# Performance work log

Measured on AMD Instinct MI355X. Metric: run time of the kernel, lower is better.

## Reference

```python
import jax, jax.numpy as jnp
import numpy as np

B, S, D = 2, 2048, 1024
HEADS, HEAD_DIM = 16, 64

def setup_inputs() -> dict:
    key = jax.random.key(0)
    ks = jax.random.split(key, 5)
    sc = 0.02
    return {
        "hidden_states": jax.random.normal(ks[0], (B, S, D), jnp.float32),
        "Wq": jax.random.normal(ks[1], (D, HEADS * HEAD_DIM), jnp.float32) * sc,
        "Wk": jax.random.normal(ks[2], (D, HEADS * HEAD_DIM), jnp.float32) * sc,
        "Wv": jax.random.normal(ks[3], (D, HEADS * HEAD_DIM), jnp.float32) * sc,
        "Wo": jax.random.normal(ks[4], (HEADS * HEAD_DIM, D), jnp.float32) * sc,
        "bo": jnp.zeros((D,), jnp.float32),
    }

def reference(hidden_states, Wq, Wk, Wv, Wo, bo):
    b, s, _ = hidden_states.shape
    # QKV projections (no bias, as in diffusers Attention defaults)
    q = (hidden_states @ Wq).reshape(b, s, HEADS, HEAD_DIM).transpose(0, 2, 1, 3)
    k = (hidden_states @ Wk).reshape(b, s, HEADS, HEAD_DIM).transpose(0, 2, 1, 3)
    v = (hidden_states @ Wv).reshape(b, s, HEADS, HEAD_DIM).transpose(0, 2, 1, 3)
    scale = 1.0 / jnp.sqrt(jnp.asarray(HEAD_DIM, hidden_states.dtype))
    scores = jnp.einsum('bhqd,bhkd->bhqk', q, k) * scale  # full NxN scores
    attn = jax.nn.softmax(scores, axis=-1)
    out = jnp.einsum('bhqk,bhkd->bhqd', attn, v)
    out = out.transpose(0, 2, 1, 3).reshape(b, s, HEADS * HEAD_DIM)
    return out @ Wo + bo
```

## Files before the change

### kernel.cpp

```cpp
#include <hip/hip_runtime.h>

#define B_ 2
#define S_ 2048
#define D_ 1024
#define H_ 16
#define HD_ 64
#define M_ (B_ * S_)

typedef __attribute__((ext_vector_type(4))) float f32x4;
typedef __attribute__((ext_vector_type(16))) float f32x16;
typedef __attribute__((ext_vector_type(8))) short s16x8;
typedef unsigned short u16;
typedef unsigned int u32;

#define QSCALE 0.1803368801111204f

__device__ __forceinline__ u16 f2bf(float f) {
  unsigned u = __float_as_uint(f);
  u += 0x7fffu + ((u >> 16) & 1u);
  return (u16)(u >> 16);
}

__device__ __forceinline__ u32 cvtpk_bf16(float lo, float hi) {
  u32 r;
  asm("v_cvt_pk_bf16_f32 %0, %1, %2" : "=v"(r) : "v"(lo), "v"(hi));
  return r;
}

__device__ __forceinline__ void g2lds16(const u16* g, u16* l) {
  __builtin_amdgcn_global_load_lds((const __attribute__((address_space(1))) u32*)(g),
                                   (__attribute__((address_space(3))) u32*)(l), 16, 0, 0);
}

__global__ __launch_bounds__(256) void prep_kernel(
    const float* __restrict__ X, const float* __restrict__ Wq,
    const float* __restrict__ Wk, const float* __restrict__ Wv,
    const float* __restrict__ Wo, u16* __restrict__ Xb, u16* __restrict__ Wt0) {
  __shared__ float tile[32][33];
  const int id = blockIdx.x;
  if (id < 4096) {
    int i = (id * 256 + threadIdx.x) * 4;
    const float4 v = *(const float4*)(X + i);
    ushort4 o;
    o.x = f2bf(v.x); o.y = f2bf(v.y); o.z = f2bf(v.z); o.w = f2bf(v.w);
    *(ushort4*)(Xb + i) = o;
    return;
  }
  const int id2 = id - 4096;
  const int z = id2 >> 10;
  const float* W = (z == 0) ? Wq : (z == 1) ? Wk : (z == 2) ? Wv : Wo;
  u16* Wt = Wt0 + (size_t)z * (D_ * D_);
  const float sc = (z == 0) ? QSCALE : 1.0f;
  const int tx = threadIdx.x & 31, ty = threadIdx.x >> 5;
  const int c0 = (id2 & 31) * 32, r0 = ((id2 >> 5) & 31) * 32;
#pragma unroll
  for (int j = 0; j < 32; j += 8)
    tile[ty + j][tx] = W[(size_t)(r0 + ty + j) * D_ + c0 + tx];
  __syncthreads();
#pragma unroll
  for (int j = 0; j < 32; j += 8)
    Wt[(size_t)(c0 + ty + j) * D_ + r0 + tx] = f2bf(tile[tx][ty + j] * sc);
}

__global__ __launch_bounds__(256) void gemm_qkv_kernel(
    const u16* __restrict__ Xb, const u16* __restrict__ WqT,
    const u16* __restrict__ WkT, const u16* __restrict__ WvT,
    u16* __restrict__ Qb, u16* __restrict__ Kb, u16* __restrict__ Vt) {
  __shared__ u16 As[2][128 * 32];
  __shared__ u16 Bs[2][128 * 32];
  const int tid = threadIdx.x;
  const int lane = tid & 63, wid = tid >> 6;
  const int wr = wid >> 1, wc = wid & 1;
  const int l15 = lane & 15, l4 = lane >> 4;
  const int bm = blockIdx.x * 128;
  const int bn128 = blockIdx.y;
  const int sel = bn128 >> 3;
  const u16* Wt = (sel == 0) ? WqT : (sel == 1) ? WkT : WvT;
  const int bn = (bn128 & 7) * 128;
  const int r0 = lane >> 2;
  const int c0 = lane & 3;

#define GSTAGE(buf, kt)                                                          \
  do {                                                                           \
    _Pragma("unroll") for (int j = 0; j < 2; ++j) {                              \
      const int row = (wid * 2 + j) * 16 + r0;                                   \
      g2lds16(Xb + (size_t)(bm + row) * D_ + (kt) + c0 * 8,                      \
              &As[buf][(wid * 2 + j) * 512]);                                    \
      g2lds16(Wt + (size_t)(bn + row) * D_ + (kt) + c0 * 8,                      \
              &Bs[buf][(wid * 2 + j) * 512]);                                    \
    }                                                                            \
  } while (0)

  f32x4 acc[4][4] = {};
  GSTAGE(0, 0);
  __syncthreads();
  int cur = 0;
  for (int kt = 0; kt < D_; kt += 32) {
    GSTAGE(cur ^ 1, (kt + 32) & (D_ - 1));
    s16x8 af[4], bfr[4];
#pragma unroll
    for (int i = 0; i < 4; ++i) af[i] = *(const s16x8*)&As[cur][(wr * 64 + i * 16 + l15) * 32 + l4 * 8];
#pragma unroll
    for (int j = 0; j < 4; ++j) bfr[j] = *(const s16x8*)&Bs[cur][(wc * 64 + j * 16 + l15) * 32 + l4 * 8];
#pragma unroll
    for (int i = 0; i < 4; ++i)
#pragma unroll
      for (int j = 0; j < 4; ++j)
        acc[i][j] = __builtin_amdgcn_mfma_f32_16x16x32_bf16(af[i], bfr[j], acc[i][j], 0, 0, 0);
    __syncthreads();
    cur ^= 1;
  }
#undef GSTAGE
#pragma unroll
  for (int i = 0; i < 4; ++i)
#pragma unroll
    for (int j = 0; j < 4; ++j)
#pragma unroll
      for (int r = 0; r < 4; ++r) {
        int m = bm + wr * 64 + i * 16 + l4 * 4 + r;
        int n = bn + wc * 64 + j * 16 + l15;
        int bb = m >> 11, s = m & (S_ - 1);
        int h = n >> 6, d = n & 63;
        u16 v = f2bf(acc[i][j][r]);
        size_t bhsel = (size_t)bb * H_ + h;
        if (sel == 0)      Qb[(bhsel * S_ + s) * HD_ + d] = v;
        else if (sel == 1) Kb[(bhsel * S_ + s) * HD_ + d] = v;
        else               Vt[(bhsel * HD_ + d) * S_ + s] = v;
      }
}

__global__ __launch_bounds__(512, 4) void attn_kernel(
    const u16* __restrict__ Qb, const u16* __restrict__ Kb,
    const u16* __restrict__ Vt, u16* __restrict__ Ob) {
  __shared__ char smem_raw[65536];
  typedef u16 (*lds_t)[2][4096];
  lds_t Ks = (lds_t)smem_raw;
  lds_t Vs = (lds_t)(smem_raw + 32768);
  const int tid = threadIdx.x;
  const int lane = tid & 63, wid = tid >> 6;
  const int qg = wid & 3, half = wid >> 2;
  const int l31 = lane & 31, hi = lane >> 5;
  const int id = blockIdx.x;
  const int bh = (id & 7) * 4 + ((id >> 3) >> 4);
  const int qx = (id >> 3) & 15;
  const size_t kbase = (size_t)bh * S_ * HD_;
  const size_t vbase = (size_t)bh * HD_ * S_;
  const int q0 = qx * 128 + qg * 32;
  const int r0 = lane >> 3;
  const int cs = ((lane & 7) ^ r0) * 8;
  const int kv0 = half << 10;

#define STAGE(buf, kvv)                                                          \
  do {                                                                           \
    _Pragma("unroll") for (int j = 0; j < 2; ++j) {                              \
      const int row = (qg * 2 + j) * 8 + r0;                                     \
      g2lds16(Kb + kbase + (size_t)((kvv) + row) * HD_ + cs,                     \
              &Ks[half][buf][(qg * 2 + j) * 512]);                               \
      g2lds16(Vt + vbase + (size_t)row * S_ + (kvv) + cs,                        \
              &Vs[half][buf][(qg * 2 + j) * 512]);                               \
    }                                                                            \
  } while (0)

  STAGE(0, kv0);

  s16x8 aq[4];
#pragma unroll
  for (int kc = 0; kc < 4; ++kc)
    aq[kc] = *(const s16x8*)(Qb + kbase + (size_t)(q0 + l31) * HD_ + kc * 16 + hi * 8);

  f32x16 acc0 = {}, acc1 = {};
  float ls = 0.f;

  __syncthreads();

  for (int t = 0; t < 16; ++t) {
    const int buf = t & 1;
    STAGE(buf ^ 1, kv0 + (((t + 1) & 15) << 6));

    f32x16 s0 = {}, s1 = {};
    __builtin_amdgcn_s_setprio(1);
#pragma unroll
    for (int kc = 0; kc < 4; ++kc) {
      const int ch = ((kc * 2 + hi) ^ (l31 & 7)) * 8;
      const s16x8 ka0 = *(const s16x8*)&Ks[half][buf][(l31) * 64 + ch];
      const s16x8 ka1 = *(const s16x8*)&Ks[half][buf][(32 + l31) * 64 + ch];
      s0 = __builtin_amdgcn_mfma_f32_32x32x16_bf16(ka0, aq[kc], s0, 0, 0, 0);
      s1 = __builtin_amdgcn_mfma_f32_32x32x16_bf16(ka1, aq[kc], s1, 0, 0, 0);
    }
    __builtin_amdgcn_s_setprio(0);

    float t0 = 0.f, t1 = 0.f;
#pragma unroll
    for (int r = 0; r < 16; ++r) {
      s0[r] = __builtin_amdgcn_exp2f(s0[r]);
      s1[r] = __builtin_amdgcn_exp2f(s1[r]);
      t0 += s0[r];
      t1 += s1[r];
    }
    ls += t0 + t1;

    s16x8 pa[4];
#pragma unroll
    for (int c = 0; c < 4; ++c) {
      const int rr = (c & 1) * 8;
      u32 a0, a1, b0, b1;
      if (c < 2) {
        a0 = cvtpk_bf16(s0[rr + 0], s0[rr + 1]);
        a1 = cvtpk_bf16(s0[rr + 2], s0[rr + 3]);
        b0 = cvtpk_bf16(s0[rr + 4], s0[rr + 5]);
        b1 = cvtpk_bf16(s0[rr + 6], s0[rr + 7]);
      } else {
        a0 = cvtpk_bf16(s1[rr + 0], s1[rr + 1]);
        a1 = cvtpk_bf16(s1[rr + 2], s1[rr + 3]);
        b0 = cvtpk_bf16(s1[rr + 4], s1[rr + 5]);
        b1 = cvtpk_bf16(s1[rr + 6], s1[rr + 7]);
      }
      asm volatile("v_permlane32_swap_b32 %0, %1" : "+v"(a0), "+v"(b0));
      asm volatile("v_permlane32_swap_b32 %0, %1" : "+v"(a1), "+v"(b1));
      union { u32 u[4]; s16x8 v; } pk;
      pk.u[0] = a0; pk.u[1] = a1; pk.u[2] = b0; pk.u[3] = b1;
      pa[c] = pk.v;
    }

    __builtin_amdgcn_s_setprio(1);
#pragma unroll
    for (int c = 0; c < 4; ++c) {
      const int ch = ((c * 2 + hi) ^ (l31 & 7)) * 8;
      const s16x8 vb0 = *(const s16x8*)&Vs[half][buf][(l31) * 64 + ch];
      const s16x8 vb1 = *(const s16x8*)&Vs[half][buf][(32 + l31) * 64 + ch];
      acc0 = __builtin_amdgcn_mfma_f32_32x32x16_bf16(pa[c], vb0, acc0, 0, 0, 0);
      acc1 = __builtin_amdgcn_mfma_f32_32x32x16_bf16(pa[c], vb1, acc1, 0, 0, 0);
    }
    __builtin_amdgcn_s_setprio(0);

    __syncthreads();
  }
#undef STAGE

  float (*MB)[64][33] = (float(*)[64][33])smem_raw;
  if (half) {
#pragma unroll
    for (int r = 0; r < 16; ++r) {
      MB[qg][lane][r] = acc0[r];
      MB[qg][lane][16 + r] = acc1[r];
    }
    MB[qg][lane][32] = ls;
  }
  __syncthreads();
  if (!half) {
#pragma unroll
    for (int r = 0; r < 16; ++r) {
      acc0[r] += MB[qg][lane][r];
      acc1[r] += MB[qg][lane][16 + r];
    }
    ls += MB[qg][lane][32];
    ls += __shfl_xor(ls, 32);
    const int bb = bh >> 4, h = bh & 15;
#pragma unroll
    for (int r = 0; r < 16; ++r) {
      const int qrow = (r & 3) + 8 * (r >> 2) + 4 * hi;
      const float rinv = 1.0f / __shfl(ls, qrow);
      const int q = q0 + qrow;
      Ob[(size_t)(bb * S_ + q) * (H_ * HD_) + h * HD_ + l31] = f2bf(acc0[r] * rinv);
      Ob[(size_t)(bb * S_ + q) * (H_ * HD_) + h * HD_ + 32 + l31] = f2bf(acc1[r] * rinv);
    }
  }
}

__global__ __launch_bounds__(256) void gemm_o_kernel(
    const u16* __restrict__ A, const u16* __restrict__ Bt,
    const float* __restrict__ bias, float* __restrict__ C) {
  __shared__ u16 As[2][128 * 32];
  __shared__ u16 Bs[2][128 * 32];
  const int tid = threadIdx.x;
  const int lane = tid & 63, wid = tid >> 6;
  const int wr = wid >> 1, wc = wid & 1;
  const int l15 = lane & 15, l4 = lane >> 4;
  const int bm = blockIdx.x * 128;
  const int bn = blockIdx.y * 128;
  const int r0 = lane >> 2;
  const int c0 = lane & 3;

#define GSTAGE(buf, kt)                                                          \
  do {                                                                           \
    _Pragma("unroll") for (int j = 0; j < 2; ++j) {                              \
      const int row = (wid * 2 + j) * 16 + r0;                                   \
      g2lds16(A + (size_t)(bm + row) * D_ + (kt) + c0 * 8,                       \
              &As[buf][(wid * 2 + j) * 512]);                                    \
      g2lds16(Bt + (size_t)(bn + row) * D_ + (kt) + c0 * 8,                      \
              &Bs[buf][(wid * 2 + j) * 512]);                                    \
    }                                                                            \
  } while (0)

  f32x4 acc[4][4] = {};
  GSTAGE(0, 0);
  __syncthreads();
  int cur = 0;
  for (int kt = 0; kt < D_; kt += 32) {
    GSTAGE(cur ^ 1, (kt + 32) & (D_ - 1));
    s16x8 af[4], bfr[4];
#pragma unroll
    for (int i = 0; i < 4; ++i) af[i] = *(const s16x8*)&As[cur][(wr * 64 + i * 16 + l15) * 32 + l4 * 8];
#pragma unroll
    for (int j = 0; j < 4; ++j) bfr[j] = *(const s16x8*)&Bs[cur][(wc * 64 + j * 16 + l15) * 32 + l4 * 8];
#pragma unroll
    for (int i = 0; i < 4; ++i)
#pragma unroll
      for (int j = 0; j < 4; ++j)
        acc[i][j] = __builtin_amdgcn_mfma_f32_16x16x32_bf16(af[i], bfr[j], acc[i][j], 0, 0, 0);
    __syncthreads();
    cur ^= 1;
  }
#undef GSTAGE
#pragma unroll
  for (int i = 0; i < 4; ++i)
#pragma unroll
    for (int j = 0; j < 4; ++j)
#pragma unroll
      for (int r = 0; r < 4; ++r) {
        int m = bm + wr * 64 + i * 16 + l4 * 4 + r;
        int n = bn + wc * 64 + j * 16 + l15;
        C[(size_t)m * D_ + n] = acc[i][j][r] + bias[n];
      }
}

extern "C" void kernel_launch(void* const* d_in, const int* in_sizes, int n_in,
                              void* d_out, int out_size, void* d_ws, size_t ws_size,
                              hipStream_t stream) {
  const float* X  = (const float*)d_in[0];
  const float* Wq = (const float*)d_in[1];
  const float* Wk = (const float*)d_in[2];
  const float* Wv = (const float*)d_in[3];
  const float* Wo = (const float*)d_in[4];
  const float* bo = (const float*)d_in[5];
  float* out = (float*)d_out;

  char* w = (char*)d_ws;
  u16* Xb  = (u16*)(w);
  u16* WT  = (u16*)(w + (8u << 20));
  u16* WqT = WT;
  u16* WkT = WT + (1u << 20);
  u16* WvT = WT + (2u << 20);
  u16* WoT = WT + (3u << 20);
  u16* Qb  = (u16*)(w + (16u << 20));
  u16* Kb  = (u16*)(w + (24u << 20));
  u16* Vt  = (u16*)(w + (32u << 20));
  u16* Ob  = (u16*)(w + (40u << 20));

  prep_kernel<<<8192, 256, 0, stream>>>(X, Wq, Wk, Wv, Wo, Xb, WT);
  gemm_qkv_kernel<<<dim3(32, 24), 256, 0, stream>>>(Xb, WqT, WkT, WvT, Qb, Kb, Vt);
  attn_kernel<<<512, 512, 0, stream>>>(Qb, Kb, Vt, Ob);
  gemm_o_kernel<<<dim3(32, 8), 256, 0, stream>>>(Ob, WoT, bo, out);
}
```

Measured before the change: 116.9 us.

## Compute softmax row sums via MFMA with ones and swizzle GEMM block mapping

The attention kernel drops the per-lane VALU sum of exponentials. It adds an extra MFMA of P against an all-ones bf16 vector, so the row sums land in the same layout as the output accumulator, which removes the shuffles in the epilogue. Both GEMM kernels switch to a 1D grid with a block-index swizzle that spreads consecutive blocks across XCDs and changes tile order for L2 locality. The LDS swizzle offsets are also hoisted into registers. The cost is one extra MFMA per four PV MFMAs, a larger merge buffer in shared memory, and row sums built from bf16-rounded probabilities.

```diff
diff --git a/kernel.cpp b/kernel.cpp
--- a/kernel.cpp
+++ b/kernel.cpp
@@ -72,8 +72,9 @@
   const int lane = tid & 63, wid = tid >> 6;
   const int wr = wid >> 1, wc = wid & 1;
   const int l15 = lane & 15, l4 = lane >> 4;
-  const int bm = blockIdx.x * 128;
-  const int bn128 = blockIdx.y;
+  const int swz = (blockIdx.x & 7) * 96 + (blockIdx.x >> 3);
+  const int bm = (swz & 31) * 128;
+  const int bn128 = swz >> 5;
   const int sel = bn128 >> 3;
   const u16* Wt = (sel == 0) ? WqT : (sel == 1) ? WkT : WvT;
   const int bn = (bn128 & 7) * 128;
@@ -168,8 +169,14 @@
   for (int kc = 0; kc < 4; ++kc)
     aq[kc] = *(const s16x8*)(Qb + kbase + (size_t)(q0 + l31) * HD_ + kc * 16 + hi * 8);
 
-  f32x16 acc0 = {}, acc1 = {};
-  float ls = 0.f;
+  const short one_bf = (short)0x3F80;
+  const s16x8 ones8 = {one_bf, one_bf, one_bf, one_bf, one_bf, one_bf, one_bf, one_bf};
+
+  f32x16 acc0 = {}, acc1 = {}, lsacc = {};
+
+  int choff[4];
+#pragma unroll
+  for (int c = 0; c < 4; ++c) choff[c] = ((c * 2 + hi) ^ (l31 & 7)) * 8;
 
   __syncthreads();
 
@@ -181,23 +188,18 @@
     __builtin_amdgcn_s_setprio(1);
 #pragma unroll
     for (int kc = 0; kc < 4; ++kc) {
-      const int ch = ((kc * 2 + hi) ^ (l31 & 7)) * 8;
-      const s16x8 ka0 = *(const s16x8*)&Ks[half][buf][(l31) * 64 + ch];
-      const s16x8 ka1 = *(const s16x8*)&Ks[half][buf][(32 + l31) * 64 + ch];
+      const s16x8 ka0 = *(const s16x8*)&Ks[half][buf][(l31) * 64 + choff[kc]];
+      const s16x8 ka1 = *(const s16x8*)&Ks[half][buf][(32 + l31) * 64 + choff[kc]];
       s0 = __builtin_amdgcn_mfma_f32_32x32x16_bf16(ka0, aq[kc], s0, 0, 0, 0);
       s1 = __builtin_amdgcn_mfma_f32_32x32x16_bf16(ka1, aq[kc], s1, 0, 0, 0);
     }
     __builtin_amdgcn_s_setprio(0);
 
-    float t0 = 0.f, t1 = 0.f;
 #pragma unroll
     for (int r = 0; r < 16; ++r) {
       s0[r] = __builtin_amdgcn_exp2f(s0[r]);
       s1[r] = __builtin_amdgcn_exp2f(s1[r]);
-      t0 += s0[r];
-      t1 += s1[r];
-    }
-    ls += t0 + t1;
+    }
 
     s16x8 pa[4];
 #pragma unroll
@@ -225,11 +227,11 @@
     __builtin_amdgcn_s_setprio(1);
 #pragma unroll
     for (int c = 0; c < 4; ++c) {
-      const int ch = ((c * 2 + hi) ^ (l31 & 7)) * 8;
-      const s16x8 vb0 = *(const s16x8*)&Vs[half][buf][(l31) * 64 + ch];
-      const s16x8 vb1 = *(const s16x8*)&Vs[half][buf][(32 + l31) * 64 + ch];
+      const s16x8 vb0 = *(const s16x8*)&Vs[half][buf][(l31) * 64 + choff[c]];
+      const s16x8 vb1 = *(const s16x8*)&Vs[half][buf][(32 + l31) * 64 + choff[c]];
       acc0 = __builtin_amdgcn_mfma_f32_32x32x16_bf16(pa[c], vb0, acc0, 0, 0, 0);
       acc1 = __builtin_amdgcn_mfma_f32_32x32x16_bf16(pa[c], vb1, acc1, 0, 0, 0);
+      lsacc = __builtin_amdgcn_mfma_f32_32x32x16_bf16(pa[c], ones8, lsacc, 0, 0, 0);
     }
     __builtin_amdgcn_s_setprio(0);
 
@@ -237,32 +239,27 @@
   }
 #undef STAGE
 
-  float (*MB)[64][33] = (float(*)[64][33])smem_raw;
+  float (*MB)[64][49] = (float(*)[64][49])smem_raw;
   if (half) {
 #pragma unroll
     for (int r = 0; r < 16; ++r) {
       MB[qg][lane][r] = acc0[r];
       MB[qg][lane][16 + r] = acc1[r];
-    }
-    MB[qg][lane][32] = ls;
+      MB[qg][lane][32 + r] = lsacc[r];
+    }
   }
   __syncthreads();
   if (!half) {
+    const int bb = bh >> 4, h = bh & 15;
 #pragma unroll
     for (int r = 0; r < 16; ++r) {
-      acc0[r] += MB[qg][lane][r];
-      acc1[r] += MB[qg][lane][16 + r];
-    }
-    ls += MB[qg][lane][32];
-    ls += __shfl_xor(ls, 32);
-    const int bb = bh >> 4, h = bh & 15;
-#pragma unroll
-    for (int r = 0; r < 16; ++r) {
+      const float o0 = acc0[r] + MB[qg][lane][r];
+      const float o1 = acc1[r] + MB[qg][lane][16 + r];
+      const float rinv = 1.0f / (lsacc[r] + MB[qg][lane][32 + r]);
       const int qrow = (r & 3) + 8 * (r >> 2) + 4 * hi;
-      const float rinv = 1.0f / __shfl(ls, qrow);
       const int q = q0 + qrow;
-      Ob[(size_t)(bb * S_ + q) * (H_ * HD_) + h * HD_ + l31] = f2bf(acc0[r] * rinv);
-      Ob[(size_t)(bb * S_ + q) * (H_ * HD_) + h * HD_ + 32 + l31] = f2bf(acc1[r] * rinv);
+      Ob[(size_t)(bb * S_ + q) * (H_ * HD_) + h * HD_ + l31] = f2bf(o0 * rinv);
+      Ob[(size_t)(bb * S_ + q) * (H_ * HD_) + h * HD_ + 32 + l31] = f2bf(o1 * rinv);
     }
   }
 }
@@ -276,8 +273,9 @@
   const int lane = tid & 63, wid = tid >> 6;
   const int wr = wid >> 1, wc = wid & 1;
   const int l15 = lane & 15, l4 = lane >> 4;
-  const int bm = blockIdx.x * 128;
-  const int bn = blockIdx.y * 128;
+  const int swz = (blockIdx.x & 7) * 32 + (blockIdx.x >> 3);
+  const int bm = (swz & 31) * 128;
+  const int bn = (swz >> 5) * 128;
   const int r0 = lane >> 2;
   const int c0 = lane & 3;
 
@@ -348,7 +346,7 @@
   u16* Ob  = (u16*)(w + (40u << 20));
 
   prep_kernel<<<8192, 256, 0, stream>>>(X, Wq, Wk, Wv, Wo, Xb, WT);
-  gemm_qkv_kernel<<<dim3(32, 24), 256, 0, stream>>>(Xb, WqT, WkT, WvT, Qb, Kb, Vt);
+  gemm_qkv_kernel<<<768, 256, 0, stream>>>(Xb, WqT, WkT, WvT, Qb, Kb, Vt);
   attn_kernel<<<512, 512, 0, stream>>>(Qb, Kb, Vt, Ob);
-  gemm_o_kernel<<<dim3(32, 8), 256, 0, stream>>>(Ob, WoT, bo, out);
-}
+  gemm_o_kernel<<<256, 256, 0, stream>>>(Ob, WoT, bo, out);
+}
```

Result: slower. 129.0 us (+10.4%).

## Fuse X fp32-to-bf16 conversion into QKV GEMM and widen N tile to 256

Applied to the files above, without the earlier changes.

Drops the separate conversion pass that wrote a bf16 copy of the hidden states. The QKV GEMM now loads fp32 X directly into registers, converts it with packed bf16 conversion instructions, and writes it to LDS. The GEMM block also grows to 512 threads with a 128x256 tile, so each converted A tile is reused across more output columns. This saves one global write/read round trip of X. The cost is register-based A staging instead of async global-to-LDS loads, half as many GEMM blocks, and more LDS per block.

```diff
diff --git a/kernel.cpp b/kernel.cpp
--- a/kernel.cpp
+++ b/kernel.cpp
@@ -33,26 +33,17 @@
 }
 
 __global__ __launch_bounds__(256) void prep_kernel(
-    const float* __restrict__ X, const float* __restrict__ Wq,
-    const float* __restrict__ Wk, const float* __restrict__ Wv,
-    const float* __restrict__ Wo, u16* __restrict__ Xb, u16* __restrict__ Wt0) {
+    const float* __restrict__ Wq, const float* __restrict__ Wk,
+    const float* __restrict__ Wv, const float* __restrict__ Wo,
+    u16* __restrict__ Wt0) {
   __shared__ float tile[32][33];
   const int id = blockIdx.x;
-  if (id < 4096) {
-    int i = (id * 256 + threadIdx.x) * 4;
-    const float4 v = *(const float4*)(X + i);
-    ushort4 o;
-    o.x = f2bf(v.x); o.y = f2bf(v.y); o.z = f2bf(v.z); o.w = f2bf(v.w);
-    *(ushort4*)(Xb + i) = o;
-    return;
-  }
-  const int id2 = id - 4096;
-  const int z = id2 >> 10;
+  const int z = id >> 10;
   const float* W = (z == 0) ? Wq : (z == 1) ? Wk : (z == 2) ? Wv : Wo;
   u16* Wt = Wt0 + (size_t)z * (D_ * D_);
   const float sc = (z == 0) ? QSCALE : 1.0f;
   const int tx = threadIdx.x & 31, ty = threadIdx.x >> 5;
-  const int c0 = (id2 & 31) * 32, r0 = ((id2 >> 5) & 31) * 32;
+  const int c0 = (id & 31) * 32, r0 = ((id >> 5) & 31) * 32;
 #pragma unroll
   for (int j = 0; j < 32; j += 8)
     tile[ty + j][tx] = W[(size_t)(r0 + ty + j) * D_ + c0 + tx];
@@ -62,41 +53,55 @@
     Wt[(size_t)(c0 + ty + j) * D_ + r0 + tx] = f2bf(tile[tx][ty + j] * sc);
 }
 
-__global__ __launch_bounds__(256) void gemm_qkv_kernel(
-    const u16* __restrict__ Xb, const u16* __restrict__ WqT,
+__global__ __launch_bounds__(512) void gemm_qkv_kernel(
+    const float* __restrict__ X, const u16* __restrict__ WqT,
     const u16* __restrict__ WkT, const u16* __restrict__ WvT,
     u16* __restrict__ Qb, u16* __restrict__ Kb, u16* __restrict__ Vt) {
   __shared__ u16 As[2][128 * 32];
-  __shared__ u16 Bs[2][128 * 32];
+  __shared__ u16 Bs[2][256 * 32];
   const int tid = threadIdx.x;
   const int lane = tid & 63, wid = tid >> 6;
-  const int wr = wid >> 1, wc = wid & 1;
+  const int wr = wid >> 2, wc = wid & 3;
   const int l15 = lane & 15, l4 = lane >> 4;
   const int bm = blockIdx.x * 128;
-  const int bn128 = blockIdx.y;
-  const int sel = bn128 >> 3;
+  const int strip = blockIdx.y;
+  const int sel = strip >> 2;
   const u16* Wt = (sel == 0) ? WqT : (sel == 1) ? WkT : WvT;
-  const int bn = (bn128 & 7) * 128;
-  const int r0 = lane >> 2;
-  const int c0 = lane & 3;
-
-#define GSTAGE(buf, kt)                                                          \
+  const int bnp = (strip & 3) * 256;
+  const int arow = tid >> 2, ac = tid & 3;
+  const float* Xa = X + (size_t)(bm + arow) * D_ + ac * 8;
+  const int brow0 = wid * 16 + (lane >> 2), bc = lane & 3;
+
+#define STAGE_B(buf, kt)                                                         \
   do {                                                                           \
-    _Pragma("unroll") for (int j = 0; j < 2; ++j) {                              \
-      const int row = (wid * 2 + j) * 16 + r0;                                   \
-      g2lds16(Xb + (size_t)(bm + row) * D_ + (kt) + c0 * 8,                      \
-              &As[buf][(wid * 2 + j) * 512]);                                    \
-      g2lds16(Wt + (size_t)(bn + row) * D_ + (kt) + c0 * 8,                      \
-              &Bs[buf][(wid * 2 + j) * 512]);                                    \
-    }                                                                            \
+    _Pragma("unroll") for (int j = 0; j < 2; ++j)                                \
+      g2lds16(Wt + (size_t)(bnp + brow0 + j * 128) * D_ + (kt) + bc * 8,         \
+              &Bs[buf][wid * 512 + j * 4096]);                                   \
   } while (0)
 
+#define LOAD_A(kt)                                                               \
+  xa = *(const float4*)(Xa + (kt));                                              \
+  xb = *(const float4*)(Xa + (kt) + 4)
+
+#define WRITE_A(buf)                                                             \
+  do {                                                                           \
+    union { u32 u[4]; s16x8 v; } pk;                                             \
+    pk.u[0] = cvtpk_bf16(xa.x, xa.y); pk.u[1] = cvtpk_bf16(xa.z, xa.w);          \
+    pk.u[2] = cvtpk_bf16(xb.x, xb.y); pk.u[3] = cvtpk_bf16(xb.z, xb.w);          \
+    *(s16x8*)&As[buf][tid * 8] = pk.v;                                           \
+  } while (0)
+
+  float4 xa, xb;
   f32x4 acc[4][4] = {};
-  GSTAGE(0, 0);
+  LOAD_A(0);
+  STAGE_B(0, 0);
+  WRITE_A(0);
   __syncthreads();
   int cur = 0;
   for (int kt = 0; kt < D_; kt += 32) {
-    GSTAGE(cur ^ 1, (kt + 32) & (D_ - 1));
+    const int nkt = (kt + 32) & (D_ - 1);
+    LOAD_A(nkt);
+    STAGE_B(cur ^ 1, nkt);
     s16x8 af[4], bfr[4];
 #pragma unroll
     for (int i = 0; i < 4; ++i) af[i] = *(const s16x8*)&As[cur][(wr * 64 + i * 16 + l15) * 32 + l4 * 8];
@@ -107,10 +112,13 @@
 #pragma unroll
       for (int j = 0; j < 4; ++j)
         acc[i][j] = __builtin_amdgcn_mfma_f32_16x16x32_bf16(af[i], bfr[j], acc[i][j], 0, 0, 0);
+    WRITE_A(cur ^ 1);
     __syncthreads();
     cur ^= 1;
   }
-#undef GSTAGE
+#undef STAGE_B
+#undef LOAD_A
+#undef WRITE_A
 #pragma unroll
   for (int i = 0; i < 4; ++i)
 #pragma unroll
@@ -118,7 +126,7 @@
 #pragma unroll
       for (int r = 0; r < 4; ++r) {
         int m = bm + wr * 64 + i * 16 + l4 * 4 + r;
-        int n = bn + wc * 64 + j * 16 + l15;
+        int n = bnp + wc * 64 + j * 16 + l15;
         int bb = m >> 11, s = m & (S_ - 1);
         int h = n >> 6, d = n & 63;
         u16 v = f2bf(acc[i][j][r]);
@@ -336,7 +344,6 @@
   float* out = (float*)d_out;
 
   char* w = (char*)d_ws;
-  u16* Xb  = (u16*)(w);
   u16* WT  = (u16*)(w + (8u << 20));
   u16* WqT = WT;
   u16* WkT = WT + (1u << 20);
@@ -347,8 +354,8 @@
   u16* Vt  = (u16*)(w + (32u << 20));
   u16* Ob  = (u16*)(w + (40u << 20));
 
-  prep_kernel<<<8192, 256, 0, stream>>>(X, Wq, Wk, Wv, Wo, Xb, WT);
-  gemm_qkv_kernel<<<dim3(32, 24), 256, 0, stream>>>(Xb, WqT, WkT, WvT, Qb, Kb, Vt);
+  prep_kernel<<<4096, 256, 0, stream>>>(Wq, Wk, Wv, Wo, WT);
+  gemm_qkv_kernel<<<dim3(32, 12), 512, 0, stream>>>(X, WqT, WkT, WvT, Qb, Kb, Vt);
   attn_kernel<<<512, 512, 0, stream>>>(Qb, Kb, Vt, Ob);
   gemm_o_kernel<<<dim3(32, 8), 256, 0, stream>>>(Ob, WoT, bo, out);
 }
```

After: 125.7 us. +7.6%, slower.

## Split attention KV halves into separate blocks, merge partials in output GEMM

Applied to the files above, without the earlier changes.

The attention kernel now launches 1024 blocks of 256 threads, each handling one KV half, instead of 512 blocks of 512 threads that reduced both halves through LDS. Each half writes unnormalized bf16 partial outputs and row sums to global buffers. The output-projection GEMM loads both partials, sums them, normalizes by the combined row sum and packs the result into LDS as its A operand. This removes the in-block reduction barrier and raises block-level parallelism, but adds an extra partial-output round trip through global memory and extra bf16 rounding. It also reuses the Xb buffer for the second partial.

```diff
diff --git a/kernel.cpp b/kernel.cpp
--- a/kernel.cpp
+++ b/kernel.cpp
@@ -19,6 +19,10 @@
   unsigned u = __float_as_uint(f);
   u += 0x7fffu + ((u >> 16) & 1u);
   return (u16)(u >> 16);
+}
+
+__device__ __forceinline__ float bf2f(short s) {
+  return __uint_as_float(((u32)(unsigned short)s) << 16);
 }
 
 __device__ __forceinline__ u32 cvtpk_bf16(float lo, float hi) {
@@ -129,23 +133,24 @@
       }
 }
 
-__global__ __launch_bounds__(512, 4) void attn_kernel(
+__global__ __launch_bounds__(256, 4) void attn_kernel(
     const u16* __restrict__ Qb, const u16* __restrict__ Kb,
-    const u16* __restrict__ Vt, u16* __restrict__ Ob) {
-  __shared__ char smem_raw[65536];
-  typedef u16 (*lds_t)[2][4096];
-  lds_t Ks = (lds_t)smem_raw;
-  lds_t Vs = (lds_t)(smem_raw + 32768);
+    const u16* __restrict__ Vt, u16* __restrict__ P0, u16* __restrict__ P1,
+    float* __restrict__ ls0, float* __restrict__ ls1) {
+  __shared__ u16 Ks[2][4096];
+  __shared__ u16 Vs[2][4096];
   const int tid = threadIdx.x;
   const int lane = tid & 63, wid = tid >> 6;
-  const int qg = wid & 3, half = wid >> 2;
   const int l31 = lane & 31, hi = lane >> 5;
   const int id = blockIdx.x;
-  const int bh = (id & 7) * 4 + ((id >> 3) >> 4);
-  const int qx = (id >> 3) & 15;
+  const int rr_ = id >> 3;
+  const int bh = (id & 7) * 4 + (rr_ >> 5);
+  const int sub = rr_ & 31;
+  const int half = sub >> 4;
+  const int qx = sub & 15;
   const size_t kbase = (size_t)bh * S_ * HD_;
   const size_t vbase = (size_t)bh * HD_ * S_;
-  const int q0 = qx * 128 + qg * 32;
+  const int q0 = qx * 128 + wid * 32;
   const int r0 = lane >> 3;
   const int cs = ((lane & 7) ^ r0) * 8;
   const int kv0 = half << 10;
@@ -153,11 +158,11 @@
 #define STAGE(buf, kvv)                                                          \
   do {                                                                           \
     _Pragma("unroll") for (int j = 0; j < 2; ++j) {                              \
-      const int row = (qg * 2 + j) * 8 + r0;                                     \
+      const int row = (wid * 2 + j) * 8 + r0;                                    \
       g2lds16(Kb + kbase + (size_t)((kvv) + row) * HD_ + cs,                     \
-              &Ks[half][buf][(qg * 2 + j) * 512]);                               \
+              &Ks[buf][(wid * 2 + j) * 512]);                                    \
       g2lds16(Vt + vbase + (size_t)row * S_ + (kvv) + cs,                        \
-              &Vs[half][buf][(qg * 2 + j) * 512]);                               \
+              &Vs[buf][(wid * 2 + j) * 512]);                                    \
     }                                                                            \
   } while (0)
 
@@ -182,8 +187,8 @@
 #pragma unroll
     for (int kc = 0; kc < 4; ++kc) {
       const int ch = ((kc * 2 + hi) ^ (l31 & 7)) * 8;
-      const s16x8 ka0 = *(const s16x8*)&Ks[half][buf][(l31) * 64 + ch];
-      const s16x8 ka1 = *(const s16x8*)&Ks[half][buf][(32 + l31) * 64 + ch];
+      const s16x8 ka0 = *(const s16x8*)&Ks[buf][(l31) * 64 + ch];
+      const s16x8 ka1 = *(const s16x8*)&Ks[buf][(32 + l31) * 64 + ch];
       s0 = __builtin_amdgcn_mfma_f32_32x32x16_bf16(ka0, aq[kc], s0, 0, 0, 0);
       s1 = __builtin_amdgcn_mfma_f32_32x32x16_bf16(ka1, aq[kc], s1, 0, 0, 0);
     }
@@ -226,8 +231,8 @@
 #pragma unroll
     for (int c = 0; c < 4; ++c) {
       const int ch = ((c * 2 + hi) ^ (l31 & 7)) * 8;
-      const s16x8 vb0 = *(const s16x8*)&Vs[half][buf][(l31) * 64 + ch];
-      const s16x8 vb1 = *(const s16x8*)&Vs[half][buf][(32 + l31) * 64 + ch];
+      const s16x8 vb0 = *(const s16x8*)&Vs[buf][(l31) * 64 + ch];
+      const s16x8 vb1 = *(const s16x8*)&Vs[buf][(32 + l31) * 64 + ch];
       acc0 = __builtin_amdgcn_mfma_f32_32x32x16_bf16(pa[c], vb0, acc0, 0, 0, 0);
       acc1 = __builtin_amdgcn_mfma_f32_32x32x16_bf16(pa[c], vb1, acc1, 0, 0, 0);
     }
@@ -237,39 +242,25 @@
   }
 #undef STAGE
 
-  float (*MB)[64][33] = (float(*)[64][33])smem_raw;
-  if (half) {
-#pragma unroll
-    for (int r = 0; r < 16; ++r) {
-      MB[qg][lane][r] = acc0[r];
-      MB[qg][lane][16 + r] = acc1[r];
-    }
-    MB[qg][lane][32] = ls;
-  }
-  __syncthreads();
-  if (!half) {
-#pragma unroll
-    for (int r = 0; r < 16; ++r) {
-      acc0[r] += MB[qg][lane][r];
-      acc1[r] += MB[qg][lane][16 + r];
-    }
-    ls += MB[qg][lane][32];
-    ls += __shfl_xor(ls, 32);
-    const int bb = bh >> 4, h = bh & 15;
-#pragma unroll
-    for (int r = 0; r < 16; ++r) {
-      const int qrow = (r & 3) + 8 * (r >> 2) + 4 * hi;
-      const float rinv = 1.0f / __shfl(ls, qrow);
-      const int q = q0 + qrow;
-      Ob[(size_t)(bb * S_ + q) * (H_ * HD_) + h * HD_ + l31] = f2bf(acc0[r] * rinv);
-      Ob[(size_t)(bb * S_ + q) * (H_ * HD_) + h * HD_ + 32 + l31] = f2bf(acc1[r] * rinv);
-    }
+  ls += __shfl_xor(ls, 32);
+  const int bb = bh >> 4, h = bh & 15;
+  u16* P = half ? P1 : P0;
+  float* LS = half ? ls1 : ls0;
+  if (hi == 0) LS[(size_t)(bb * S_ + q0 + l31) * H_ + h] = ls;
+#pragma unroll
+  for (int r = 0; r < 16; ++r) {
+    const int qrow = (r & 3) + 8 * (r >> 2) + 4 * hi;
+    const int q = q0 + qrow;
+    P[(size_t)(bb * S_ + q) * (H_ * HD_) + h * HD_ + l31] = f2bf(acc0[r]);
+    P[(size_t)(bb * S_ + q) * (H_ * HD_) + h * HD_ + 32 + l31] = f2bf(acc1[r]);
   }
 }
 
 __global__ __launch_bounds__(256) void gemm_o_kernel(
-    const u16* __restrict__ A, const u16* __restrict__ Bt,
-    const float* __restrict__ bias, float* __restrict__ C) {
+    const u16* __restrict__ P0, const u16* __restrict__ P1,
+    const float* __restrict__ ls0, const float* __restrict__ ls1,
+    const u16* __restrict__ Bt, const float* __restrict__ bias,
+    float* __restrict__ C) {
   __shared__ u16 As[2][128 * 32];
   __shared__ u16 Bs[2][128 * 32];
   const int tid = threadIdx.x;
@@ -280,24 +271,54 @@
   const int bn = blockIdx.y * 128;
   const int r0 = lane >> 2;
   const int c0 = lane & 3;
-
-#define GSTAGE(buf, kt)                                                          \
+  const int arow0 = (wid * 2) * 16 + r0, arow1 = (wid * 2 + 1) * 16 + r0;
+
+#define STAGE_B(buf, kt)                                                         \
   do {                                                                           \
     _Pragma("unroll") for (int j = 0; j < 2; ++j) {                              \
       const int row = (wid * 2 + j) * 16 + r0;                                   \
-      g2lds16(A + (size_t)(bm + row) * D_ + (kt) + c0 * 8,                       \
-              &As[buf][(wid * 2 + j) * 512]);                                    \
       g2lds16(Bt + (size_t)(bn + row) * D_ + (kt) + c0 * 8,                      \
               &Bs[buf][(wid * 2 + j) * 512]);                                    \
     }                                                                            \
   } while (0)
 
+#define LOAD_M(kt)                                                               \
+  do {                                                                           \
+    const int col = (kt) + c0 * 8, hh = col >> 6;                                \
+    ma0 = *(const s16x8*)&P0[(size_t)(bm + arow0) * D_ + col];                   \
+    mb0 = *(const s16x8*)&P1[(size_t)(bm + arow0) * D_ + col];                   \
+    ma1 = *(const s16x8*)&P0[(size_t)(bm + arow1) * D_ + col];                   \
+    mb1 = *(const s16x8*)&P1[(size_t)(bm + arow1) * D_ + col];                   \
+    lsv0 = ls0[(size_t)(bm + arow0) * H_ + hh] + ls1[(size_t)(bm + arow0) * H_ + hh]; \
+    lsv1 = ls0[(size_t)(bm + arow1) * H_ + hh] + ls1[(size_t)(bm + arow1) * H_ + hh]; \
+  } while (0)
+
+#define WRITE_M(buf)                                                             \
+  do {                                                                           \
+    const float ri0 = 1.0f / lsv0, ri1 = 1.0f / lsv1;                            \
+    union { u32 u[4]; s16x8 v; } pk0, pk1;                                       \
+    _Pragma("unroll") for (int e = 0; e < 4; ++e) {                              \
+      pk0.u[e] = cvtpk_bf16((bf2f(ma0[2 * e]) + bf2f(mb0[2 * e])) * ri0,         \
+                            (bf2f(ma0[2 * e + 1]) + bf2f(mb0[2 * e + 1])) * ri0);\
+      pk1.u[e] = cvtpk_bf16((bf2f(ma1[2 * e]) + bf2f(mb1[2 * e])) * ri1,         \
+                            (bf2f(ma1[2 * e + 1]) + bf2f(mb1[2 * e + 1])) * ri1);\
+    }                                                                            \
+    *(s16x8*)&As[buf][arow0 * 32 + c0 * 8] = pk0.v;                              \
+    *(s16x8*)&As[buf][arow1 * 32 + c0 * 8] = pk1.v;                              \
+  } while (0)
+
+  s16x8 ma0, mb0, ma1, mb1;
+  float lsv0, lsv1;
   f32x4 acc[4][4] = {};
-  GSTAGE(0, 0);
+  LOAD_M(0);
+  STAGE_B(0, 0);
+  WRITE_M(0);
   __syncthreads();
   int cur = 0;
   for (int kt = 0; kt < D_; kt += 32) {
-    GSTAGE(cur ^ 1, (kt + 32) & (D_ - 1));
+    const int nkt = (kt + 32) & (D_ - 1);
+    LOAD_M(nkt);
+    STAGE_B(cur ^ 1, nkt);
     s16x8 af[4], bfr[4];
 #pragma unroll
     for (int i = 0; i < 4; ++i) af[i] = *(const s16x8*)&As[cur][(wr * 64 + i * 16 + l15) * 32 + l4 * 8];
@@ -308,10 +329,13 @@
 #pragma unroll
       for (int j = 0; j < 4; ++j)
         acc[i][j] = __builtin_amdgcn_mfma_f32_16x16x32_bf16(af[i], bfr[j], acc[i][j], 0, 0, 0);
+    WRITE_M(cur ^ 1);
     __syncthreads();
     cur ^= 1;
   }
-#undef GSTAGE
+#undef STAGE_B
+#undef LOAD_M
+#undef WRITE_M
 #pragma unroll
   for (int i = 0; i < 4; ++i)
 #pragma unroll
@@ -345,10 +369,13 @@
   u16* Qb  = (u16*)(w + (16u << 20));
   u16* Kb  = (u16*)(w + (24u << 20));
   u16* Vt  = (u16*)(w + (32u << 20));
-  u16* Ob  = (u16*)(w + (40u << 20));
+  u16* P0  = (u16*)(w + (40u << 20));
+  u16* P1  = Xb;
+  float* ls0 = (float*)(w + (48u << 20));
+  float* ls1 = (float*)(w + (48u << 20) + (256u << 10));
 
   prep_kernel<<<8192, 256, 0, stream>>>(X, Wq, Wk, Wv, Wo, Xb, WT);
   gemm_qkv_kernel<<<dim3(32, 24), 256, 0, stream>>>(Xb, WqT, WkT, WvT, Qb, Kb, Vt);
-  attn_kernel<<<512, 512, 0, stream>>>(Qb, Kb, Vt, Ob);
-  gemm_o_kernel<<<dim3(32, 8), 256, 0, stream>>>(Ob, WoT, bo, out);
-}
+  attn_kernel<<<1024, 256, 0, stream>>>(Qb, Kb, Vt, P0, P1, ls0, ls1);
+  gemm_o_kernel<<<dim3(32, 8), 256, 0, stream>>>(P0, P1, ls0, ls1, WoT, bo, out);
+}
```

Measured after the change: 134.9 us. +15.4%, slower.
